# Optimization experiments

Measured on AMD Instinct MI355X. Metric: run time of the kernel, lower is better.

Reference implementation:

```python
import jax, jax.numpy as jnp
import numpy as np

N_NODES = 50000


def _sage_conv(x, src, dst, Wl, bl, Wr):
    # mean aggregation of neighbor (source) features at destination nodes
    msg = x[src]                                              # [E, d]
    agg = jax.ops.segment_sum(msg, dst, num_segments=N_NODES)  # [N, d]
    cnt = jax.ops.segment_sum(jnp.ones((src.shape[0],), x.dtype), dst,
                              num_segments=N_NODES)            # [N]
    agg = agg / jnp.clip(cnt, 1.0)[:, None]
    # lin_l(aggregated) + lin_r(self), bias only on lin_l (PyG default)
    return agg @ Wl + bl + x @ Wr


def setup_inputs() -> dict:
    key = jax.random.key(0)
    ks = jax.random.split(key, 8)
    d = 128
    E = 800000
    x = jax.random.normal(ks[0], (N_NODES, d), dtype=jnp.float32)
    edge_index = jax.random.randint(ks[1], (2, E), 0, N_NODES, dtype=jnp.int64)
    s1 = 1.0 / np.sqrt(d)
    s2 = 1.0 / np.sqrt(32)
    return {
        "x": x,
        "edge_index": edge_index,
        "W1l": jax.random.normal(ks[2], (d, 32), jnp.float32) * s1,
        "b1": jnp.zeros((32,), jnp.float32),
        "W1r": jax.random.normal(ks[3], (d, 32), jnp.float32) * s1,
        "W2l": jax.random.normal(ks[4], (32, 32), jnp.float32) * s2,
        "b2": jnp.zeros((32,), jnp.float32),
        "W2r": jax.random.normal(ks[5], (32, 32), jnp.float32) * s2,
    }


def reference(x, edge_index, W1l, b1, W1r, W2l, b2, W2r):
    src, dst = edge_index[0], edge_index[1]
    h = jax.nn.relu(_sage_conv(x, src, dst, W1l, b1, W1r))
    return _sage_conv(h, src, dst, W2l, b2, W2r)
```

## Files before the change

### kernel.cpp

```cpp
#include <hip/hip_runtime.h>


#define N_NODES 50000
#define NB 782
#define BKS 64
#define GB 256
#define CAPE 1280
#define TILE 3200

__global__ __launch_bounds__(256) void k_front(
    const float* __restrict__ in, const float* __restrict__ Wl,
    const float* __restrict__ Wr, float* __restrict__ z, int N, int K,
    const int* __restrict__ src, const int* __restrict__ dst,
    int* __restrict__ gcnt, int* __restrict__ ebuf, int E) {
  __shared__ union {
    struct { float xs[64 * 68]; float ws[64 * 64]; } p;
    struct { unsigned pe[TILE]; int hist[NB]; int cur[NB]; } b;
  } sm;
  const int t = threadIdx.x;

  if (blockIdx.x < GB) {
    const int chunk = (E + GB - 1) / GB;
    const int e0 = blockIdx.x * chunk;
    int e1 = e0 + chunk;
    if (e1 > E) e1 = E;
    for (int ts = e0; ts < e1; ts += TILE) {
      int te = ts + TILE;
      if (te > e1) te = e1;
      const int n = te - ts;
      for (int i = t; i < NB; i += 256) sm.b.hist[i] = 0;
      __syncthreads();
      for (int i = t; i < n; i += 256) {
        unsigned s = (unsigned)src[ts + i];
        unsigned d = (unsigned)dst[ts + i];
        sm.b.pe[i] = (s << 16) | d;
        atomicAdd(&sm.b.hist[d >> 6], 1);
      }
      __syncthreads();
      for (int c = t; c < NB; c += 256) {
        int h = sm.b.hist[c];
        sm.b.cur[c] = h ? atomicAdd(&gcnt[c], h) : 0;
      }
      __syncthreads();
      for (int i = t; i < n; i += 256) {
        unsigned pe = sm.b.pe[i];
        int d = (int)(pe & 0xFFFFu);
        int s = (int)(pe >> 16);
        int c = d >> 6;
        int p = atomicAdd(&sm.b.cur[c], 1);
        if (p < CAPE) ebuf[(size_t)c * CAPE + p] = (s << 6) | (d & 63);
      }
      __syncthreads();
    }
    return;
  }

  const int n0 = (blockIdx.x - GB) * 64;
  const int nvalid = (N - n0) < 64 ? (N - n0) : 64;
  const int tx = t & 15, ty = t >> 4;
  const int c0 = tx * 4;
  const int nl = ty * 4;

  float acc[4][4];
#pragma unroll
  for (int i = 0; i < 4; i++)
#pragma unroll
    for (int j = 0; j < 4; j++) acc[i][j] = 0.f;

  for (int kc = 0; kc < K; kc += 64) {
    const int KC = (K - kc) < 64 ? (K - kc) : 64;
    for (int i = t; i < KC * 32; i += 256) {
      int k = i >> 5, c = i & 31;
      sm.p.ws[k * 64 + c] = Wl[(size_t)(kc + k) * 32 + c];
      sm.p.ws[k * 64 + 32 + c] = Wr[(size_t)(kc + k) * 32 + c];
    }
    {
      const int kq = KC >> 2;
      const int sh = (KC == 64) ? 4 : 3;
      const int lim = nvalid * kq;
      for (int i = t; i < lim; i += 256) {
        int n = i >> sh, q = i & (kq - 1);
        float4 v = *(const float4*)(in + (size_t)(n0 + n) * K + kc + q * 4);
        *(float4*)(sm.p.xs + n * 68 + q * 4) = v;
      }
    }
    __syncthreads();

    const float* x0 = sm.p.xs + (nl + 0) * 68;
    const float* x1 = sm.p.xs + (nl + 1) * 68;
    const float* x2 = sm.p.xs + (nl + 2) * 68;
    const float* x3 = sm.p.xs + (nl + 3) * 68;
    for (int k = 0; k < KC; k += 4) {
      float4 xa = *(const float4*)(x0 + k);
      float4 xb = *(const float4*)(x1 + k);
      float4 xc = *(const float4*)(x2 + k);
      float4 xd = *(const float4*)(x3 + k);
#pragma unroll
      for (int kk = 0; kk < 4; kk++) {
        float4 w = *(const float4*)(sm.p.ws + (k + kk) * 64 + c0);
        float va = ((const float*)&xa)[kk];
        float vb = ((const float*)&xb)[kk];
        float vc = ((const float*)&xc)[kk];
        float vd = ((const float*)&xd)[kk];
        acc[0][0] += va * w.x; acc[0][1] += va * w.y;
        acc[0][2] += va * w.z; acc[0][3] += va * w.w;
        acc[1][0] += vb * w.x; acc[1][1] += vb * w.y;
        acc[1][2] += vb * w.z; acc[1][3] += vb * w.w;
        acc[2][0] += vc * w.x; acc[2][1] += vc * w.y;
        acc[2][2] += vc * w.z; acc[2][3] += vc * w.w;
        acc[3][0] += vd * w.x; acc[3][1] += vd * w.y;
        acc[3][2] += vd * w.z; acc[3][3] += vd * w.w;
      }
    }
    __syncthreads();
  }
#pragma unroll
  for (int i = 0; i < 4; i++) {
    int node = n0 + nl + i;
    if (node < N) {
      float4 v = make_float4(acc[i][0], acc[i][1], acc[i][2], acc[i][3]);
      *(float4*)(z + (size_t)node * 64 + c0) = v;
    }
  }
}

#define SORT_PHASE(EBUF, NE)                                         \
  for (int i = t; i < (NE); i += 512) lds_e[i] = (EBUF)[base + i];   \
  if (t < BKS) deg[t] = 0;                                           \
  __syncthreads();                                                   \
  for (int i = t; i < (NE); i += 512) atomicAdd(&deg[lds_e[i] & 63], 1); \
  __syncthreads();                                                   \
  if (t < 64) {                                                      \
    int d = deg[t];                                                  \
    int x = d;                                                       \
    _Pragma("unroll") for (int o = 1; o < 64; o <<= 1) {             \
      int y = __shfl_up(x, o, 64);                                   \
      if (t >= o) x += y;                                            \
    }                                                                \
    off[t] = x - d;                                                  \
    cur[t] = x - d;                                                  \
  }                                                                  \
  __syncthreads();                                                   \
  for (int i = t; i < (NE); i += 512) {                              \
    int v = lds_e[i];                                                \
    int p = atomicAdd(&cur[v & 63], 1);                              \
    lds_s[p] = v >> 6;                                               \
  }                                                                  \
  __syncthreads();

__global__ __launch_bounds__(512) void k_fagg1(
    const float* __restrict__ zc, const int* __restrict__ ebuf,
    const int* __restrict__ gcnt, const float* __restrict__ b1,
    const float* __restrict__ W2l, const float* __restrict__ W2r,
    float* __restrict__ z2, int N) {
  __shared__ int lds_e[CAPE];
  __shared__ int lds_s[CAPE];
  __shared__ int deg[BKS];
  __shared__ int cur[BKS];
  __shared__ int off[BKS];
  __shared__ float w2p[32 * 64];
  __shared__ __align__(16) float bsh[32];
  __shared__ __align__(16) float hbuf[BKS * 36];
  const int t = threadIdx.x;
  const int k = blockIdx.x;
  int ne = gcnt[k];
  if (ne > CAPE) ne = CAPE;
  const size_t base = (size_t)k * CAPE;

  for (int i = t; i < 2048; i += 512) {
    int jj = i >> 6, c = i & 63;
    w2p[i] = (c < 32) ? W2l[jj * 32 + c] : W2r[jj * 32 + (c - 32)];
  }
  if (t < 32) bsh[t] = b1[t];

  SORT_PHASE(ebuf, ne)

  const float4* zc4 = (const float4*)zc;
  const int w = t >> 6, l = t & 63;
  const int es = l >> 3, fi = l & 7;
  const int n0 = k << 6;
  const int w8 = w * 8;
#pragma unroll
  for (int p = 0; p < 8; p += 2) {
    const int nA = w8 + p, nB = w8 + p + 1;
    const int aA = off[nA], dA = deg[nA];
    const int aB = off[nB], dB = deg[nB];
    float4 accA = make_float4(0.f, 0.f, 0.f, 0.f);
    float4 accB = make_float4(0.f, 0.f, 0.f, 0.f);
    const int mx = dA > dB ? dA : dB;
    for (int eb = 0; eb < mx; eb += 8) {
      const int i = eb + es;
      if (i < dA) {
        float4 f = zc4[(size_t)lds_s[aA + i] * 16 + fi];
        accA.x += f.x; accA.y += f.y; accA.z += f.z; accA.w += f.w;
      }
      if (i < dB) {
        float4 f = zc4[(size_t)lds_s[aB + i] * 16 + fi];
        accB.x += f.x; accB.y += f.y; accB.z += f.z; accB.w += f.w;
      }
    }
#pragma unroll
    for (int m = 8; m < 64; m <<= 1) {
      accA.x += __shfl_xor(accA.x, m, 64);
      accA.y += __shfl_xor(accA.y, m, 64);
      accA.z += __shfl_xor(accA.z, m, 64);
      accA.w += __shfl_xor(accA.w, m, 64);
      accB.x += __shfl_xor(accB.x, m, 64);
      accB.y += __shfl_xor(accB.y, m, 64);
      accB.z += __shfl_xor(accB.z, m, 64);
      accB.w += __shfl_xor(accB.w, m, 64);
    }
    if (es == 0) {
      const float4 b4 = *(const float4*)(bsh + fi * 4);
      if (n0 + nA < N) {
        const float rdA = 1.0f / (float)(dA > 1 ? dA : 1);
        const float4 sA = *(const float4*)(zc + (size_t)(n0 + nA) * 64 + 32 + fi * 4);
        float4 h;
        h.x = fmaxf(accA.x * rdA + b4.x + sA.x, 0.f);
        h.y = fmaxf(accA.y * rdA + b4.y + sA.y, 0.f);
        h.z = fmaxf(accA.z * rdA + b4.z + sA.z, 0.f);
        h.w = fmaxf(accA.w * rdA + b4.w + sA.w, 0.f);
        *(float4*)(hbuf + nA * 36 + fi * 4) = h;
      }
      if (n0 + nB < N) {
        const float rdB = 1.0f / (float)(dB > 1 ? dB : 1);
        const float4 sB = *(const float4*)(zc + (size_t)(n0 + nB) * 64 + 32 + fi * 4);
        float4 h;
        h.x = fmaxf(accB.x * rdB + b4.x + sB.x, 0.f);
        h.y = fmaxf(accB.y * rdB + b4.y + sB.y, 0.f);
        h.z = fmaxf(accB.z * rdB + b4.z + sB.z, 0.f);
        h.w = fmaxf(accB.w * rdB + b4.w + sB.w, 0.f);
        *(float4*)(hbuf + nB * 36 + fi * 4) = h;
      }
    }
  }
  __syncthreads();

  const int g = t >> 5, j = t & 31;
#pragma unroll
  for (int i = 0; i < 4; i++) {
    const int nl = g * 4 + i;
    const int node = n0 + nl;
    if (node >= N) break;
    const float h = hbuf[nl * 36 + j];
    float p0 = 0.f, p1 = 0.f;
#pragma unroll
    for (int jj = 0; jj < 32; jj++) {
      float hj = __shfl(h, jj, 32);
      p0 += hj * w2p[jj * 64 + j];
      p1 += hj * w2p[jj * 64 + 32 + j];
    }
    z2[(size_t)node * 64 + j] = p0;
    z2[(size_t)node * 64 + 32 + j] = p1;
  }
}

__global__ __launch_bounds__(512) void k_fagg2(
    const float* __restrict__ z2, const int* __restrict__ ebuf,
    const int* __restrict__ gcnt, const float* __restrict__ b2,
    float* __restrict__ out, int N) {
  __shared__ int lds_e[CAPE];
  __shared__ int lds_s[CAPE];
  __shared__ int deg[BKS];
  __shared__ int cur[BKS];
  __shared__ int off[BKS];
  __shared__ __align__(16) float bsh[32];
  const int t = threadIdx.x;
  const int k = blockIdx.x;
  int ne = gcnt[k];
  if (ne > CAPE) ne = CAPE;
  const size_t base = (size_t)k * CAPE;

  if (t < 32) bsh[t] = b2[t];

  SORT_PHASE(ebuf, ne)

  const float4* z24 = (const float4*)z2;
  const int w = t >> 6, l = t & 63;
  const int es = l >> 3, fi = l & 7;
  const int n0 = k << 6;
  const int w8 = w * 8;
#pragma unroll
  for (int p = 0; p < 8; p += 2) {
    const int nA = w8 + p, nB = w8 + p + 1;
    const int aA = off[nA], dA = deg[nA];
    const int aB = off[nB], dB = deg[nB];
    float4 accA = make_float4(0.f, 0.f, 0.f, 0.f);
    float4 accB = make_float4(0.f, 0.f, 0.f, 0.f);
    const int mx = dA > dB ? dA : dB;
    for (int eb = 0; eb < mx; eb += 8) {
      const int i = eb + es;
      if (i < dA) {
        float4 f = z24[(size_t)lds_s[aA + i] * 16 + fi];
        accA.x += f.x; accA.y += f.y; accA.z += f.z; accA.w += f.w;
      }
      if (i < dB) {
        float4 f = z24[(size_t)lds_s[aB + i] * 16 + fi];
        accB.x += f.x; accB.y += f.y; accB.z += f.z; accB.w += f.w;
      }
    }
#pragma unroll
    for (int m = 8; m < 64; m <<= 1) {
      accA.x += __shfl_xor(accA.x, m, 64);
      accA.y += __shfl_xor(accA.y, m, 64);
      accA.z += __shfl_xor(accA.z, m, 64);
      accA.w += __shfl_xor(accA.w, m, 64);
      accB.x += __shfl_xor(accB.x, m, 64);
      accB.y += __shfl_xor(accB.y, m, 64);
      accB.z += __shfl_xor(accB.z, m, 64);
      accB.w += __shfl_xor(accB.w, m, 64);
    }
    if (es == 0) {
      const float4 b4 = *(const float4*)(bsh + fi * 4);
      if (n0 + nA < N) {
        const float rdA = 1.0f / (float)(dA > 1 ? dA : 1);
        const float4 sA = *(const float4*)(z2 + (size_t)(n0 + nA) * 64 + 32 + fi * 4);
        float4 o;
        o.x = accA.x * rdA + b4.x + sA.x;
        o.y = accA.y * rdA + b4.y + sA.y;
        o.z = accA.z * rdA + b4.z + sA.z;
        o.w = accA.w * rdA + b4.w + sA.w;
        *(float4*)(out + (size_t)(n0 + nA) * 32 + fi * 4) = o;
      }
      if (n0 + nB < N) {
        const float rdB = 1.0f / (float)(dB > 1 ? dB : 1);
        const float4 sB = *(const float4*)(z2 + (size_t)(n0 + nB) * 64 + 32 + fi * 4);
        float4 o;
        o.x = accB.x * rdB + b4.x + sB.x;
        o.y = accB.y * rdB + b4.y + sB.y;
        o.z = accB.z * rdB + b4.z + sB.z;
        o.w = accB.w * rdB + b4.w + sB.w;
        *(float4*)(out + (size_t)(n0 + nB) * 32 + fi * 4) = o;
      }
    }
  }
}

extern "C" void kernel_launch(void* const* d_in, const int* in_sizes, int n_in,
                              void* d_out, int out_size, void* d_ws,
                              size_t ws_size, hipStream_t stream) {
  const float* x = (const float*)d_in[0];
  const int* ei = (const int*)d_in[1];
  const float* W1l = (const float*)d_in[2];
  const float* b1 = (const float*)d_in[3];
  const float* W1r = (const float*)d_in[4];
  const float* W2l = (const float*)d_in[5];
  const float* b2 = (const float*)d_in[6];
  const float* W2r = (const float*)d_in[7];
  float* out = (float*)d_out;

  const int N = N_NODES;
  const int E = in_sizes[1] / 2;

  float* zc = (float*)d_ws;
  float* zc2 = zc + (size_t)N * 64;
  int* ebuf = (int*)(zc2 + (size_t)N * 64);
  int* gcnt = ebuf + (size_t)NB * CAPE;

  const int* srcp = ei;
  const int* dstp = ei + E;

  const int nblk_proj = (N + 63) / 64;

  hipMemsetAsync(gcnt, 0, NB * sizeof(int), stream);
  k_front<<<GB + nblk_proj, 256, 0, stream>>>(x, W1l, W1r, zc, N, 128, srcp,
                                              dstp, gcnt, ebuf, E);
  k_fagg1<<<NB, 512, 0, stream>>>(zc, ebuf, gcnt, b1, W2l, W2r, zc2, N);
  k_fagg2<<<NB, 512, 0, stream>>>(zc2, ebuf, gcnt, b2, out, N);
}
```

Measured before the change: 169.2 us.

## Split projected features into separate lin_l/lin_r arrays and vectorize edge loads

Stores the lin_l and lin_r projections in separate 32-wide arrays, so each neighbor gather reads a dense 128-byte row instead of half of a 256-byte row. Edge src/dst reads and bucket loads into LDS now use int4 vector loads, with the per-block chunk rounded up to a multiple of 4 to keep those loads aligned. The global bucket counters are padded 32 ints apart to avoid atomic contention on shared cache lines. The workspace grows slightly for the padded counters, and the chunk rounding relies on tail handling being correct.

```diff
diff --git a/kernel.cpp b/kernel.cpp
--- a/kernel.cpp
+++ b/kernel.cpp
@@ -10,17 +10,18 @@
 
 __global__ __launch_bounds__(256) void k_front(
     const float* __restrict__ in, const float* __restrict__ Wl,
-    const float* __restrict__ Wr, float* __restrict__ z, int N, int K,
-    const int* __restrict__ src, const int* __restrict__ dst,
-    int* __restrict__ gcnt, int* __restrict__ ebuf, int E) {
-  __shared__ union {
+    const float* __restrict__ Wr, float* __restrict__ zl,
+    float* __restrict__ zr, int N, int K, const int* __restrict__ src,
+    const int* __restrict__ dst, int* __restrict__ gcnt,
+    int* __restrict__ ebuf, int E) {
+  __shared__ __align__(16) union {
     struct { float xs[64 * 68]; float ws[64 * 64]; } p;
     struct { unsigned pe[TILE]; int hist[NB]; int cur[NB]; } b;
   } sm;
   const int t = threadIdx.x;
 
   if (blockIdx.x < GB) {
-    const int chunk = (E + GB - 1) / GB;
+    const int chunk = (((E + GB - 1) / GB) + 3) & ~3;
     const int e0 = blockIdx.x * chunk;
     int e1 = e0 + chunk;
     if (e1 > E) e1 = E;
@@ -28,18 +29,38 @@
       int te = ts + TILE;
       if (te > e1) te = e1;
       const int n = te - ts;
+      if (n <= 0) break;
       for (int i = t; i < NB; i += 256) sm.b.hist[i] = 0;
       __syncthreads();
-      for (int i = t; i < n; i += 256) {
-        unsigned s = (unsigned)src[ts + i];
-        unsigned d = (unsigned)dst[ts + i];
-        sm.b.pe[i] = (s << 16) | d;
-        atomicAdd(&sm.b.hist[d >> 6], 1);
+      {
+        const int n4 = n >> 2;
+        const int4* s4 = (const int4*)(src + ts);
+        const int4* d4 = (const int4*)(dst + ts);
+        for (int i = t; i < n4; i += 256) {
+          int4 sv = s4[i];
+          int4 dv = d4[i];
+          int4 pk;
+          pk.x = (sv.x << 16) | dv.x;
+          pk.y = (sv.y << 16) | dv.y;
+          pk.z = (sv.z << 16) | dv.z;
+          pk.w = (sv.w << 16) | dv.w;
+          *(int4*)(sm.b.pe + 4 * i) = pk;
+          atomicAdd(&sm.b.hist[dv.x >> 6], 1);
+          atomicAdd(&sm.b.hist[dv.y >> 6], 1);
+          atomicAdd(&sm.b.hist[dv.z >> 6], 1);
+          atomicAdd(&sm.b.hist[dv.w >> 6], 1);
+        }
+        for (int i = (n4 << 2) + t; i < n; i += 256) {
+          unsigned s = (unsigned)src[ts + i];
+          unsigned d = (unsigned)dst[ts + i];
+          sm.b.pe[i] = (s << 16) | d;
+          atomicAdd(&sm.b.hist[d >> 6], 1);
+        }
       }
       __syncthreads();
       for (int c = t; c < NB; c += 256) {
         int h = sm.b.hist[c];
-        sm.b.cur[c] = h ? atomicAdd(&gcnt[c], h) : 0;
+        sm.b.cur[c] = h ? atomicAdd(&gcnt[c * 32], h) : 0;
       }
       __syncthreads();
       for (int i = t; i < n; i += 256) {
@@ -119,41 +140,54 @@
     int node = n0 + nl + i;
     if (node < N) {
       float4 v = make_float4(acc[i][0], acc[i][1], acc[i][2], acc[i][3]);
-      *(float4*)(z + (size_t)node * 64 + c0) = v;
+      if (c0 < 32)
+        *(float4*)(zl + (size_t)node * 32 + c0) = v;
+      else
+        *(float4*)(zr + (size_t)node * 32 + (c0 - 32)) = v;
     }
   }
 }
 
-#define SORT_PHASE(EBUF, NE)                                         \
-  for (int i = t; i < (NE); i += 512) lds_e[i] = (EBUF)[base + i];   \
-  if (t < BKS) deg[t] = 0;                                           \
-  __syncthreads();                                                   \
+#define SORT_PHASE(EBUF, NE)                                             \
+  {                                                                      \
+    const int ne4 = (NE) >> 2;                                           \
+    const int4* eb4 = (const int4*)((EBUF) + base);                      \
+    for (int i = t; i < ne4; i += 512) {                                 \
+      int4 v = eb4[i];                                                   \
+      *(int4*)(lds_e + 4 * i) = v;                                       \
+    }                                                                    \
+    for (int i = (ne4 << 2) + t; i < (NE); i += 512)                     \
+      lds_e[i] = (EBUF)[base + i];                                       \
+  }                                                                      \
+  if (t < BKS) deg[t] = 0;                                               \
+  __syncthreads();                                                       \
   for (int i = t; i < (NE); i += 512) atomicAdd(&deg[lds_e[i] & 63], 1); \
-  __syncthreads();                                                   \
-  if (t < 64) {                                                      \
-    int d = deg[t];                                                  \
-    int x = d;                                                       \
-    _Pragma("unroll") for (int o = 1; o < 64; o <<= 1) {             \
-      int y = __shfl_up(x, o, 64);                                   \
-      if (t >= o) x += y;                                            \
-    }                                                                \
-    off[t] = x - d;                                                  \
-    cur[t] = x - d;                                                  \
-  }                                                                  \
-  __syncthreads();                                                   \
-  for (int i = t; i < (NE); i += 512) {                              \
-    int v = lds_e[i];                                                \
-    int p = atomicAdd(&cur[v & 63], 1);                              \
-    lds_s[p] = v >> 6;                                               \
-  }                                                                  \
+  __syncthreads();                                                       \
+  if (t < 64) {                                                          \
+    int d = deg[t];                                                      \
+    int x = d;                                                           \
+    _Pragma("unroll") for (int o = 1; o < 64; o <<= 1) {                 \
+      int y = __shfl_up(x, o, 64);                                       \
+      if (t >= o) x += y;                                                \
+    }                                                                    \
+    off[t] = x - d;                                                      \
+    cur[t] = x - d;                                                      \
+  }                                                                      \
+  __syncthreads();                                                       \
+  for (int i = t; i < (NE); i += 512) {                                  \
+    int v = lds_e[i];                                                    \
+    int p = atomicAdd(&cur[v & 63], 1);                                  \
+    lds_s[p] = v >> 6;                                                   \
+  }                                                                      \
   __syncthreads();
 
 __global__ __launch_bounds__(512) void k_fagg1(
-    const float* __restrict__ zc, const int* __restrict__ ebuf,
-    const int* __restrict__ gcnt, const float* __restrict__ b1,
-    const float* __restrict__ W2l, const float* __restrict__ W2r,
-    float* __restrict__ z2, int N) {
-  __shared__ int lds_e[CAPE];
+    const float* __restrict__ zl, const float* __restrict__ zr,
+    const int* __restrict__ ebuf, const int* __restrict__ gcnt,
+    const float* __restrict__ b1, const float* __restrict__ W2l,
+    const float* __restrict__ W2r, float* __restrict__ z2l,
+    float* __restrict__ z2r, int N) {
+  __shared__ __align__(16) int lds_e[CAPE];
   __shared__ int lds_s[CAPE];
   __shared__ int deg[BKS];
   __shared__ int cur[BKS];
@@ -163,7 +197,7 @@
   __shared__ __align__(16) float hbuf[BKS * 36];
   const int t = threadIdx.x;
   const int k = blockIdx.x;
-  int ne = gcnt[k];
+  int ne = gcnt[k * 32];
   if (ne > CAPE) ne = CAPE;
   const size_t base = (size_t)k * CAPE;
 
@@ -175,7 +209,7 @@
 
   SORT_PHASE(ebuf, ne)
 
-  const float4* zc4 = (const float4*)zc;
+  const float4* zl4 = (const float4*)zl;
   const int w = t >> 6, l = t & 63;
   const int es = l >> 3, fi = l & 7;
   const int n0 = k << 6;
@@ -191,11 +225,11 @@
     for (int eb = 0; eb < mx; eb += 8) {
       const int i = eb + es;
       if (i < dA) {
-        float4 f = zc4[(size_t)lds_s[aA + i] * 16 + fi];
+        float4 f = zl4[(size_t)lds_s[aA + i] * 8 + fi];
         accA.x += f.x; accA.y += f.y; accA.z += f.z; accA.w += f.w;
       }
       if (i < dB) {
-        float4 f = zc4[(size_t)lds_s[aB + i] * 16 + fi];
+        float4 f = zl4[(size_t)lds_s[aB + i] * 8 + fi];
         accB.x += f.x; accB.y += f.y; accB.z += f.z; accB.w += f.w;
       }
     }
@@ -214,7 +248,7 @@
       const float4 b4 = *(const float4*)(bsh + fi * 4);
       if (n0 + nA < N) {
         const float rdA = 1.0f / (float)(dA > 1 ? dA : 1);
-        const float4 sA = *(const float4*)(zc + (size_t)(n0 + nA) * 64 + 32 + fi * 4);
+        const float4 sA = *(const float4*)(zr + (size_t)(n0 + nA) * 32 + fi * 4);
         float4 h;
         h.x = fmaxf(accA.x * rdA + b4.x + sA.x, 0.f);
         h.y = fmaxf(accA.y * rdA + b4.y + sA.y, 0.f);
@@ -224,7 +258,7 @@
       }
       if (n0 + nB < N) {
         const float rdB = 1.0f / (float)(dB > 1 ? dB : 1);
-        const float4 sB = *(const float4*)(zc + (size_t)(n0 + nB) * 64 + 32 + fi * 4);
+        const float4 sB = *(const float4*)(zr + (size_t)(n0 + nB) * 32 + fi * 4);
         float4 h;
         h.x = fmaxf(accB.x * rdB + b4.x + sB.x, 0.f);
         h.y = fmaxf(accB.y * rdB + b4.y + sB.y, 0.f);
@@ -250,16 +284,16 @@
       p0 += hj * w2p[jj * 64 + j];
       p1 += hj * w2p[jj * 64 + 32 + j];
     }
-    z2[(size_t)node * 64 + j] = p0;
-    z2[(size_t)node * 64 + 32 + j] = p1;
+    z2l[(size_t)node * 32 + j] = p0;
+    z2r[(size_t)node * 32 + j] = p1;
   }
 }
 
 __global__ __launch_bounds__(512) void k_fagg2(
-    const float* __restrict__ z2, const int* __restrict__ ebuf,
-    const int* __restrict__ gcnt, const float* __restrict__ b2,
-    float* __restrict__ out, int N) {
-  __shared__ int lds_e[CAPE];
+    const float* __restrict__ z2l, const float* __restrict__ z2r,
+    const int* __restrict__ ebuf, const int* __restrict__ gcnt,
+    const float* __restrict__ b2, float* __restrict__ out, int N) {
+  __shared__ __align__(16) int lds_e[CAPE];
   __shared__ int lds_s[CAPE];
   __shared__ int deg[BKS];
   __shared__ int cur[BKS];
@@ -267,7 +301,7 @@
   __shared__ __align__(16) float bsh[32];
   const int t = threadIdx.x;
   const int k = blockIdx.x;
-  int ne = gcnt[k];
+  int ne = gcnt[k * 32];
   if (ne > CAPE) ne = CAPE;
   const size_t base = (size_t)k * CAPE;
 
@@ -275,7 +309,7 @@
 
   SORT_PHASE(ebuf, ne)
 
-  const float4* z24 = (const float4*)z2;
+  const float4* z24 = (const float4*)z2l;
   const int w = t >> 6, l = t & 63;
   const int es = l >> 3, fi = l & 7;
   const int n0 = k << 6;
@@ -291,11 +325,11 @@
     for (int eb = 0; eb < mx; eb += 8) {
       const int i = eb + es;
       if (i < dA) {
-        float4 f = z24[(size_t)lds_s[aA + i] * 16 + fi];
+        float4 f = z24[(size_t)lds_s[aA + i] * 8 + fi];
         accA.x += f.x; accA.y += f.y; accA.z += f.z; accA.w += f.w;
       }
       if (i < dB) {
-        float4 f = z24[(size_t)lds_s[aB + i] * 16 + fi];
+        float4 f = z24[(size_t)lds_s[aB + i] * 8 + fi];
         accB.x += f.x; accB.y += f.y; accB.z += f.z; accB.w += f.w;
       }
     }
@@ -314,7 +348,7 @@
       const float4 b4 = *(const float4*)(bsh + fi * 4);
       if (n0 + nA < N) {
         const float rdA = 1.0f / (float)(dA > 1 ? dA : 1);
-        const float4 sA = *(const float4*)(z2 + (size_t)(n0 + nA) * 64 + 32 + fi * 4);
+        const float4 sA = *(const float4*)(z2r + (size_t)(n0 + nA) * 32 + fi * 4);
         float4 o;
         o.x = accA.x * rdA + b4.x + sA.x;
         o.y = accA.y * rdA + b4.y + sA.y;
@@ -324,7 +358,7 @@
       }
       if (n0 + nB < N) {
         const float rdB = 1.0f / (float)(dB > 1 ? dB : 1);
-        const float4 sB = *(const float4*)(z2 + (size_t)(n0 + nB) * 64 + 32 + fi * 4);
+        const float4 sB = *(const float4*)(z2r + (size_t)(n0 + nB) * 32 + fi * 4);
         float4 o;
         o.x = accB.x * rdB + b4.x + sB.x;
         o.y = accB.y * rdB + b4.y + sB.y;
@@ -352,9 +386,11 @@
   const int N = N_NODES;
   const int E = in_sizes[1] / 2;
 
-  float* zc = (float*)d_ws;
-  float* zc2 = zc + (size_t)N * 64;
-  int* ebuf = (int*)(zc2 + (size_t)N * 64);
+  float* zl = (float*)d_ws;
+  float* zr = zl + (size_t)N * 32;
+  float* z2l = zr + (size_t)N * 32;
+  float* z2r = z2l + (size_t)N * 32;
+  int* ebuf = (int*)(z2r + (size_t)N * 32);
   int* gcnt = ebuf + (size_t)NB * CAPE;
 
   const int* srcp = ei;
@@ -362,9 +398,10 @@
 
   const int nblk_proj = (N + 63) / 64;
 
-  hipMemsetAsync(gcnt, 0, NB * sizeof(int), stream);
-  k_front<<<GB + nblk_proj, 256, 0, stream>>>(x, W1l, W1r, zc, N, 128, srcp,
-                                              dstp, gcnt, ebuf, E);
-  k_fagg1<<<NB, 512, 0, stream>>>(zc, ebuf, gcnt, b1, W2l, W2r, zc2, N);
-  k_fagg2<<<NB, 512, 0, stream>>>(zc2, ebuf, gcnt, b2, out, N);
+  hipMemsetAsync(gcnt, 0, (size_t)NB * 32 * sizeof(int), stream);
+  k_front<<<GB + nblk_proj, 256, 0, stream>>>(x, W1l, W1r, zl, zr, N, 128,
+                                              srcp, dstp, gcnt, ebuf, E);
+  k_fagg1<<<NB, 512, 0, stream>>>(zl, zr, ebuf, gcnt, b1, W2l, W2r, z2l, z2r,
+                                  N);
+  k_fagg2<<<NB, 512, 0, stream>>>(z2l, z2r, ebuf, gcnt, b2, out, N);
 }
```

Result: no change. 170.7 us (+0.9%).
